# Performance work log

Hardware: AMD Instinct MI355X
Metric: run time of the kernel (lower is better)

## Reference

```python
import jax, jax.numpy as jnp
import numpy as np

BETA = 0.25
K = 4096


def setup_inputs() -> dict:
    key = jax.random.key(0)
    k1, k2 = jax.random.split(key)
    z = jax.random.normal(k1, (32, 256, 32, 32), dtype=jnp.float32)
    # matches torch init: uniform(-1/k, 1/k)
    embedding = jax.random.uniform(k2, (K, 256), dtype=jnp.float32,
                                   minval=-1.0 / K, maxval=1.0 / K)
    return {"z": z, "embedding": embedding}


def reference(z, embedding):
    b, d, h, w = z.shape
    k = embedding.shape[0]
    # (b d h w) -> (n d)
    z_flat = jnp.transpose(z, (0, 2, 3, 1)).reshape(-1, d)
    # squared euclidean distances, (n, k)
    distances = (jnp.sum(z_flat * z_flat, axis=-1, keepdims=True)
                 + jnp.sum(embedding * embedding, axis=-1)
                 - 2.0 * jnp.einsum('nd,kd->nk', z_flat, embedding))
    encoding_indices = jnp.argmin(distances, axis=1)
    encodings_onehot = jax.nn.one_hot(encoding_indices, k, dtype=z.dtype)
    zq_flat = embedding[encoding_indices]
    z_quantized = jnp.transpose(zq_flat.reshape(b, h, w, d), (0, 3, 1, 2))
    loss_encoder = jnp.mean((jax.lax.stop_gradient(z_quantized) - z) ** 2)
    loss_codebook = jnp.mean((z_quantized - jax.lax.stop_gradient(z)) ** 2)
    loss = BETA * loss_encoder + loss_codebook
    # straight-through estimator
    z_quantized_st = z + jax.lax.stop_gradient(z_quantized - z)
    # perplexity of codebook usage
    enc_mean = jnp.mean(encodings_onehot, axis=0)
    perplexity = jnp.exp(-jnp.sum(enc_mean * jnp.log(enc_mean + 1e-10)))
    return (z_quantized_st, loss, perplexity, encodings_onehot,
            encoding_indices, distances)
```

## Files before the change

### kernel.cpp

```cpp
#include <hip/hip_runtime.h>
#include <hip/hip_bf16.h>

typedef unsigned short u16;
typedef unsigned int u32;
typedef unsigned long long u64;
typedef __attribute__((ext_vector_type(8))) short bf16x8;
typedef __attribute__((ext_vector_type(4))) float f32x4;

#define NROWS 32768
#define KCODES 4096
#define DDIM 256
#define HW 1024
#define ZSTRIDE_B 262144ULL

#define OFF_ZQ   0ULL
#define OFF_LOSS 8388608ULL
#define OFF_PERP 8388609ULL
#define OFF_OH   8388610ULL
#define OFF_IDX  142606338ULL
#define OFF_DIST 142639106ULL

#define T_ZH 16777280ULL
#define T_EH 25165888ULL

#define WS_IDX    0
#define WS_COUNTS 131072
#define WS_EN2    147456
#define WS_ZN2    163840
#define WS_PART   294912
#define WS_BDIST  295424
#define WS_BMIN   524288

__global__ __launch_bounds__(64) void k_prep_e_en2(const float* __restrict__ emb,
                                                   float* __restrict__ en2,
                                                   u16* __restrict__ Ehh) {
    int k = blockIdx.x;
    int l = threadIdx.x;
    float4 v = *(const float4*)(emb + (size_t)k * DDIM + l * 4);
    float s = v.x * v.x + v.y * v.y + v.z * v.z + v.w * v.w;
    #pragma unroll
    for (int m = 32; m; m >>= 1) s += __shfl_xor(s, m);
    if (l == 0) en2[k] = s;
    float vv[4] = {v.x, v.y, v.z, v.w};
    u16 ho[4];
    #pragma unroll
    for (int j = 0; j < 4; ++j) {
        __hip_bfloat16 hb = __float2bfloat16(vv[j]);
        ho[j] = *(u16*)&hb;
    }
    *(ushort4*)(Ehh + (size_t)k * DDIM + l * 4) = make_ushort4(ho[0], ho[1], ho[2], ho[3]);
}

__global__ __launch_bounds__(256) void k_zn2(const float* __restrict__ z,
                                             float* __restrict__ zn2) {
    int n = blockIdx.x * 256 + threadIdx.x;
    int b = n >> 10, hw = n & 1023;
    const float* zp = z + (size_t)b * ZSTRIDE_B + hw;
    float s = 0.f;
    #pragma unroll 8
    for (int d = 0; d < DDIM; ++d) {
        float v = zp[(size_t)d * HW];
        s = fmaf(v, v, s);
    }
    zn2[n] = s;
}

__global__ __launch_bounds__(256) void k_prep_z(const float* __restrict__ z,
                                                u16* __restrict__ Zhh) {
    __shared__ float t[32][132];
    const int tid = threadIdx.x;
    const int h0 = blockIdx.x * 128, d0 = blockIdx.y * 32, b = blockIdx.z;
    const float* zp = z + (size_t)b * ZSTRIDE_B;
    {
        int hq = (tid & 31) << 2;
        int dr = tid >> 5;
        #pragma unroll
        for (int p = 0; p < 4; ++p) {
            int d = p * 8 + dr;
            float4 v = *(const float4*)(zp + (size_t)(d0 + d) * HW + h0 + hq);
            *(float4*)&t[d][hq] = v;
        }
    }
    __syncthreads();
    {
        int nr = tid >> 1;
        int half = tid & 1;
        int n = b * HW + h0 + nr;
        u16 hv[16];
        #pragma unroll
        for (int i = 0; i < 16; ++i) {
            float v = t[half * 16 + i][nr];
            __hip_bfloat16 hb = __float2bfloat16(v);
            hv[i] = *(u16*)&hb;
        }
        u16* dst = Zhh + (size_t)n * DDIM + d0 + half * 16;
        #pragma unroll
        for (int q = 0; q < 4; ++q)
            *(ushort4*)(dst + q * 4) = *(ushort4*)&hv[q * 4];
    }
}

__global__ __launch_bounds__(256) void k_dist_mfma(
    const u16* __restrict__ Zhh, const u16* __restrict__ Ehh,
    const float* __restrict__ zn2, const float* __restrict__ en2,
    float* __restrict__ dist, float* __restrict__ bmin)
{
    __shared__ __align__(16) u16 smem[16384];
    u16* As = smem;
    u16* Bs = smem + 8192;
    float* Ct = (float*)smem;

    const int tid = threadIdx.x;
    const int w = tid >> 6, l = tid & 63;
    const int n0 = blockIdx.x * 128, k0 = blockIdx.y * 128;
    const int kb = blockIdx.y;
    const int wr = w >> 1, wc = w & 1;

    int goff[4], loff[4];
    #pragma unroll
    for (int it = 0; it < 4; ++it) {
        int o = (it << 12) + (w << 10) + (l << 4);
        int r = o >> 7;
        int c16 = (o >> 4) & 7;
        int gs = c16 ^ (r & 7);
        goff[it] = r * DDIM + gs * 8;
        loff[it] = (it << 11) + (w << 9);
    }

    f32x4 acc[4][4];
    #pragma unroll
    for (int m = 0; m < 4; ++m)
        #pragma unroll
        for (int n = 0; n < 4; ++n)
            acc[m][n] = (f32x4){0.f, 0.f, 0.f, 0.f};

    const int lr = l & 15, ks = l >> 4;
    const int ra = wr * 64 + lr, rb = wc * 64 + lr;

    const u16* Ap = Zhh + (size_t)n0 * DDIM;
    const u16* Bp = Ehh + (size_t)k0 * DDIM;
    for (int st = 0; st < 4; ++st) {
        const int d0 = st * 64;
        #pragma unroll
        for (int it = 0; it < 4; ++it) {
            __builtin_amdgcn_global_load_lds(
                (const __attribute__((address_space(1))) void*)(Ap + d0 + goff[it]),
                (__attribute__((address_space(3))) void*)(As + loff[it]), 16, 0, 0);
            __builtin_amdgcn_global_load_lds(
                (const __attribute__((address_space(1))) void*)(Bp + d0 + goff[it]),
                (__attribute__((address_space(3))) void*)(Bs + loff[it]), 16, 0, 0);
        }
        __syncthreads();
        #pragma unroll
        for (int kk = 0; kk < 2; ++kk) {
            bf16x8 af[4], bfr[4];
            #pragma unroll
            for (int m = 0; m < 4; ++m) {
                int rr = ra + m * 16;
                af[m] = *(const bf16x8*)&As[rr * 64 + ((kk * 4 + ks) ^ (rr & 7)) * 8];
            }
            #pragma unroll
            for (int n = 0; n < 4; ++n) {
                int rr = rb + n * 16;
                bfr[n] = *(const bf16x8*)&Bs[rr * 64 + ((kk * 4 + ks) ^ (rr & 7)) * 8];
            }
            #pragma unroll
            for (int m = 0; m < 4; ++m)
                #pragma unroll
                for (int n = 0; n < 4; ++n)
                    acc[m][n] = __builtin_amdgcn_mfma_f32_16x16x32_bf16(
                        af[m], bfr[n], acc[m][n], 0, 0, 0);
        }
        __syncthreads();
    }

    float ev[4];
    #pragma unroll
    for (int n = 0; n < 4; ++n) ev[n] = en2[k0 + wc * 64 + n * 16 + lr];

    #pragma unroll
    for (int m = 0; m < 4; ++m) {
        #pragma unroll
        for (int r = 0; r < 4; ++r) {
            int row = n0 + wr * 64 + m * 16 + ks * 4 + r;
            float t = zn2[row];
            int ridx = wr * 16 + ks * 4 + r;
            float rm = 3.4e38f;
            #pragma unroll
            for (int n = 0; n < 4; ++n) {
                float s  = __fadd_rn(t, ev[n]);
                float m2 = __fmul_rn(2.0f, acc[m][n][r]);
                float dv = __fsub_rn(s, m2);
                Ct[ridx * 132 + wc * 64 + n * 16 + lr] = dv;
                rm = fminf(rm, dv);
            }
            #pragma unroll
            for (int msk = 1; msk < 16; msk <<= 1)
                rm = fminf(rm, __shfl_xor(rm, msk));
            if (lr == 0)
                bmin[((size_t)row * 32 + kb) * 2 + wc] = rm;
        }
        __syncthreads();
        #pragma unroll
        for (int rr = 0; rr < 8; ++rr) {
            int rid = w * 8 + rr;
            int grow = n0 + m * 16 + (rid >> 4) * 64 + (rid & 15);
            float a = Ct[rid * 132 + l * 2];
            float b = Ct[rid * 132 + l * 2 + 1];
            *(float2*)(dist + (size_t)grow * KCODES + k0 + l * 2) = make_float2(a, b);
        }
        __syncthreads();
    }
}

__global__ __launch_bounds__(256) void k_select(
    const float* __restrict__ dist, const float* __restrict__ z,
    const float* __restrict__ emb, const float* __restrict__ zn2,
    const float* __restrict__ en2, const float* __restrict__ bmin,
    u32* __restrict__ idxarr, float* __restrict__ bdist)
{
    const int l = threadIdx.x & 63;
    const int row = blockIdx.x * 4 + (threadIdx.x >> 6);
    float bm = bmin[(size_t)row * 64 + l];
    float mn = bm;
    #pragma unroll
    for (int m = 1; m < 64; m <<= 1) mn = fminf(mn, __shfl_xor(mn, m));
    const float thr = mn + 1e-3f;
    u64 qual = __ballot(bm <= thr);

    const int b = row >> 10, hw = row & 1023;
    const float* zp = z + (size_t)b * ZSTRIDE_B + hw;
    float z0 = zp[(size_t)(l * 4 + 0) * HW];
    float z1 = zp[(size_t)(l * 4 + 1) * HW];
    float z2 = zp[(size_t)(l * 4 + 2) * HW];
    float z3 = zp[(size_t)(l * 4 + 3) * HW];
    const float zr = zn2[row];

    u64 best = ~0ull;
    int prev_kb = -1;
    u64 qq = qual;
    while (qq) {
        int bit = __ffsll(qq) - 1; qq &= qq - 1;
        int kb = bit >> 1;
        if (kb == prev_kb) continue;
        prev_kb = kb;
        const float* dr = dist + (size_t)row * KCODES + kb * 128;
        float2 d2 = *(const float2*)(dr + l * 2);
        u64 c0 = __ballot(d2.x <= thr);
        u64 c1 = __ballot(d2.y <= thr);
        u64 any = c0 | c1;
        while (any) {
            int src = __ffsll(any) - 1; any &= any - 1;
            #pragma unroll
            for (int e = 0; e < 2; ++e) {
                u64 msk = e ? c1 : c0;
                if (!((msk >> src) & 1)) continue;
                int k = kb * 128 + src * 2 + e;
                float4 e4 = *(const float4*)(emb + (size_t)k * DDIM + l * 4);
                float p = 0.f;
                p = fmaf(z0, e4.x, p);
                p = fmaf(z1, e4.y, p);
                p = fmaf(z2, e4.z, p);
                p = fmaf(z3, e4.w, p);
                #pragma unroll
                for (int m = 1; m < 64; m <<= 1) p += __shfl_xor(p, m);
                float dh = __fsub_rn(__fadd_rn(zr, en2[k]), __fmul_rn(2.0f, p));
                u32 ub = __float_as_uint(dh);
                ub = (ub & 0x80000000u) ? ~ub : (ub | 0x80000000u);
                u64 cand = ((u64)ub << 32) | (u32)k;
                best = cand < best ? cand : best;
            }
        }
    }
    if (l == 0) {
        idxarr[row] = (u32)(best & 0xffffffffu);
        u32 ub = (u32)(best >> 32);
        u32 fb = (ub & 0x80000000u) ? (ub & 0x7fffffffu) : ~ub;
        bdist[row] = __uint_as_float(fb);
    }
}

__global__ __launch_bounds__(256) void k_zq(const float* __restrict__ emb,
                                            const u32* __restrict__ idxarr,
                                            const float* __restrict__ bdist,
                                            unsigned* __restrict__ counts,
                                            float* __restrict__ out,
                                            float* __restrict__ partials) {
    int n = blockIdx.x * 256 + threadIdx.x;
    unsigned idx = idxarr[n];
    out[OFF_IDX + n] = (float)idx;
    atomicAdd(counts + idx, 1u);
    int b = n >> 10, hw = n & 1023;
    const float* ep = emb + (size_t)idx * DDIM;
    float* oq = out + OFF_ZQ + (size_t)b * ZSTRIDE_B + hw;
    #pragma unroll 2
    for (int d = 0; d < DDIM; d += 4) {
        float4 e4 = *(const float4*)(ep + d);
        oq[(size_t)(d + 0) * HW] = e4.x;
        oq[(size_t)(d + 1) * HW] = e4.y;
        oq[(size_t)(d + 2) * HW] = e4.z;
        oq[(size_t)(d + 3) * HW] = e4.w;
    }
    __shared__ float red[256];
    red[threadIdx.x] = bdist[n];
    __syncthreads();
    for (int st = 128; st > 0; st >>= 1) {
        if (threadIdx.x < st) red[threadIdx.x] += red[threadIdx.x + st];
        __syncthreads();
    }
    if (threadIdx.x == 0) partials[blockIdx.x] = red[0];
}

__global__ __launch_bounds__(256) void k_onehot(const u32* __restrict__ idxarr,
                                                const unsigned* __restrict__ counts,
                                                const float* __restrict__ partials,
                                                float* __restrict__ out) {
    const int l = threadIdx.x & 63;
    const int n = blockIdx.x * 4 + (threadIdx.x >> 6);
    const int idx = (int)idxarr[n];
    float* base = out + OFF_OH + (size_t)n * KCODES;
    #pragma unroll
    for (int i = 0; i < 16; ++i) {
        int c0 = i * 256 + l * 4;
        float2 a, b2;
        a.x  = (idx == c0)     ? 1.0f : 0.0f;
        a.y  = (idx == c0 + 1) ? 1.0f : 0.0f;
        b2.x = (idx == c0 + 2) ? 1.0f : 0.0f;
        b2.y = (idx == c0 + 3) ? 1.0f : 0.0f;
        *(float2*)(base + c0) = a;
        *(float2*)(base + c0 + 2) = b2;
    }
    if (blockIdx.x == 0) {
        __shared__ float red[256];
        int t = threadIdx.x;
        red[t] = (t < 128) ? partials[t] : 0.f;
        __syncthreads();
        for (int st = 128; st > 0; st >>= 1) {
            if (t < st) red[t] += red[t + st];
            __syncthreads();
        }
        float loss = 1.25f * (red[0] / 8388608.0f);
        __syncthreads();
        float h = 0.f;
        for (int k = t; k < KCODES; k += 256) {
            float p = (float)counts[k] * (1.0f / 32768.0f);
            h -= p * logf(p + 1e-10f);
        }
        red[t] = h;
        __syncthreads();
        for (int st = 128; st > 0; st >>= 1) {
            if (t < st) red[t] += red[t + st];
            __syncthreads();
        }
        if (t == 0) {
            out[OFF_LOSS] = loss;
            out[OFF_PERP] = expf(red[0]);
        }
    }
}

extern "C" void kernel_launch(void* const* d_in, const int* in_sizes, int n_in,
                              void* d_out, int out_size, void* d_ws, size_t ws_size,
                              hipStream_t stream) {
    (void)in_sizes; (void)n_in; (void)out_size; (void)ws_size;
    const float* z = (const float*)d_in[0];
    const float* emb = (const float*)d_in[1];
    float* out = (float*)d_out;
    char* ws = (char*)d_ws;
    u32* idxarr = (u32*)(ws + WS_IDX);
    unsigned* counts = (unsigned*)(ws + WS_COUNTS);
    float* en2 = (float*)(ws + WS_EN2);
    float* zn2 = (float*)(ws + WS_ZN2);
    float* partials = (float*)(ws + WS_PART);
    float* bdist = (float*)(ws + WS_BDIST);
    float* bmin = (float*)(ws + WS_BMIN);

    u16* Zhh = (u16*)(out + T_ZH);
    u16* Ehh = (u16*)(out + T_EH);
    float* dist = out + OFF_DIST;

    (void)hipMemsetAsync(counts, 0, (size_t)KCODES * 4, stream);

    k_prep_z<<<dim3(8, 8, 32), 256, 0, stream>>>(z, Zhh);
    k_prep_e_en2<<<KCODES, 64, 0, stream>>>(emb, en2, Ehh);
    k_zn2<<<NROWS / 256, 256, 0, stream>>>(z, zn2);
    k_dist_mfma<<<dim3(NROWS / 128, KCODES / 128), 256, 0, stream>>>(
        Zhh, Ehh, zn2, en2, dist, bmin);
    k_select<<<NROWS / 4, 256, 0, stream>>>(dist, z, emb, zn2, en2, bmin,
                                            idxarr, bdist);
    k_zq<<<NROWS / 256, 256, 0, stream>>>(emb, idxarr, bdist, counts, out, partials);
    k_onehot<<<NROWS / 4, 256, 0, stream>>>(idxarr, counts, partials, out);
}
```

Measured before the change: 554.6 us.

## Keep Z tile resident in LDS across four codebook panels and overlap epilogue

Each block of the distance GEMM now loads its full 128x256 Z tile into LDS once and loops over four 128-code panels, so Z is fetched from global memory a quarter as often and the grid shrinks to a quarter of its former size. The previous panel's epilogue is issued after the next panel's first B loads, overlapping distance writes with loads. The epilogue now writes distances straight to global memory from MFMA registers instead of staging them through LDS for coalesced float2 stores. This gives less coalesced stores and uses 80KB of LDS per block, which limits occupancy.

```diff
diff --git a/kernel.cpp b/kernel.cpp
--- a/kernel.cpp
+++ b/kernel.cpp
@@ -100,98 +100,28 @@
     }
 }
 
-__global__ __launch_bounds__(256) void k_dist_mfma(
-    const u16* __restrict__ Zhh, const u16* __restrict__ Ehh,
-    const float* __restrict__ zn2, const float* __restrict__ en2,
-    float* __restrict__ dist, float* __restrict__ bmin)
+static __device__ __forceinline__ void do_epilogue(
+    f32x4 (&acc)[4][4], const float* zrow, const float* __restrict__ en2,
+    float* __restrict__ dist, float* __restrict__ bmin,
+    int n0, int kpan, int kb, int wr, int wc, int lr, int ks)
 {
-    __shared__ __align__(16) u16 smem[16384];
-    u16* As = smem;
-    u16* Bs = smem + 8192;
-    float* Ct = (float*)smem;
-
-    const int tid = threadIdx.x;
-    const int w = tid >> 6, l = tid & 63;
-    const int n0 = blockIdx.x * 128, k0 = blockIdx.y * 128;
-    const int kb = blockIdx.y;
-    const int wr = w >> 1, wc = w & 1;
-
-    int goff[4], loff[4];
-    #pragma unroll
-    for (int it = 0; it < 4; ++it) {
-        int o = (it << 12) + (w << 10) + (l << 4);
-        int r = o >> 7;
-        int c16 = (o >> 4) & 7;
-        int gs = c16 ^ (r & 7);
-        goff[it] = r * DDIM + gs * 8;
-        loff[it] = (it << 11) + (w << 9);
-    }
-
-    f32x4 acc[4][4];
-    #pragma unroll
-    for (int m = 0; m < 4; ++m)
-        #pragma unroll
-        for (int n = 0; n < 4; ++n)
-            acc[m][n] = (f32x4){0.f, 0.f, 0.f, 0.f};
-
-    const int lr = l & 15, ks = l >> 4;
-    const int ra = wr * 64 + lr, rb = wc * 64 + lr;
-
-    const u16* Ap = Zhh + (size_t)n0 * DDIM;
-    const u16* Bp = Ehh + (size_t)k0 * DDIM;
-    for (int st = 0; st < 4; ++st) {
-        const int d0 = st * 64;
-        #pragma unroll
-        for (int it = 0; it < 4; ++it) {
-            __builtin_amdgcn_global_load_lds(
-                (const __attribute__((address_space(1))) void*)(Ap + d0 + goff[it]),
-                (__attribute__((address_space(3))) void*)(As + loff[it]), 16, 0, 0);
-            __builtin_amdgcn_global_load_lds(
-                (const __attribute__((address_space(1))) void*)(Bp + d0 + goff[it]),
-                (__attribute__((address_space(3))) void*)(Bs + loff[it]), 16, 0, 0);
-        }
-        __syncthreads();
-        #pragma unroll
-        for (int kk = 0; kk < 2; ++kk) {
-            bf16x8 af[4], bfr[4];
-            #pragma unroll
-            for (int m = 0; m < 4; ++m) {
-                int rr = ra + m * 16;
-                af[m] = *(const bf16x8*)&As[rr * 64 + ((kk * 4 + ks) ^ (rr & 7)) * 8];
-            }
-            #pragma unroll
-            for (int n = 0; n < 4; ++n) {
-                int rr = rb + n * 16;
-                bfr[n] = *(const bf16x8*)&Bs[rr * 64 + ((kk * 4 + ks) ^ (rr & 7)) * 8];
-            }
-            #pragma unroll
-            for (int m = 0; m < 4; ++m)
-                #pragma unroll
-                for (int n = 0; n < 4; ++n)
-                    acc[m][n] = __builtin_amdgcn_mfma_f32_16x16x32_bf16(
-                        af[m], bfr[n], acc[m][n], 0, 0, 0);
-        }
-        __syncthreads();
-    }
-
     float ev[4];
     #pragma unroll
-    for (int n = 0; n < 4; ++n) ev[n] = en2[k0 + wc * 64 + n * 16 + lr];
-
+    for (int n = 0; n < 4; ++n) ev[n] = en2[kpan + wc * 64 + n * 16 + lr];
     #pragma unroll
     for (int m = 0; m < 4; ++m) {
         #pragma unroll
         for (int r = 0; r < 4; ++r) {
             int row = n0 + wr * 64 + m * 16 + ks * 4 + r;
-            float t = zn2[row];
-            int ridx = wr * 16 + ks * 4 + r;
+            float t = zrow[m * 4 + r];
+            float* dp = dist + (size_t)row * KCODES + kpan + wc * 64 + lr;
             float rm = 3.4e38f;
             #pragma unroll
             for (int n = 0; n < 4; ++n) {
                 float s  = __fadd_rn(t, ev[n]);
                 float m2 = __fmul_rn(2.0f, acc[m][n][r]);
                 float dv = __fsub_rn(s, m2);
-                Ct[ridx * 132 + wc * 64 + n * 16 + lr] = dv;
+                dp[n * 16] = dv;
                 rm = fminf(rm, dv);
             }
             #pragma unroll
@@ -200,17 +130,103 @@
             if (lr == 0)
                 bmin[((size_t)row * 32 + kb) * 2 + wc] = rm;
         }
-        __syncthreads();
-        #pragma unroll
-        for (int rr = 0; rr < 8; ++rr) {
-            int rid = w * 8 + rr;
-            int grow = n0 + m * 16 + (rid >> 4) * 64 + (rid & 15);
-            float a = Ct[rid * 132 + l * 2];
-            float b = Ct[rid * 132 + l * 2 + 1];
-            *(float2*)(dist + (size_t)grow * KCODES + k0 + l * 2) = make_float2(a, b);
-        }
-        __syncthreads();
-    }
+        #pragma unroll
+        for (int n = 0; n < 4; ++n) acc[m][n] = (f32x4){0.f, 0.f, 0.f, 0.f};
+    }
+}
+
+__global__ __launch_bounds__(256) void k_dist_mfma(
+    const u16* __restrict__ Zhh, const u16* __restrict__ Ehh,
+    const float* __restrict__ zn2, const float* __restrict__ en2,
+    float* __restrict__ dist, float* __restrict__ bmin)
+{
+    __shared__ __align__(16) u16 As[32768];
+    __shared__ __align__(16) u16 Bs[8192];
+
+    const int tid = threadIdx.x;
+    const int w = tid >> 6, l = tid & 63;
+    const int n0 = blockIdx.x * 128;
+    const int kbase = blockIdx.y * 512;
+    const int wr = w >> 1, wc = w & 1;
+    const int lr = l & 15, ks = l >> 4;
+    const int ra = wr * 64 + lr, rb = wc * 64 + lr;
+
+    int goff[4], loff[4];
+    #pragma unroll
+    for (int it = 0; it < 4; ++it) {
+        int o = (it << 12) + (w << 10) + (l << 4);
+        int r = o >> 7;
+        int gs = ((o >> 4) & 7) ^ (r & 7);
+        goff[it] = r * DDIM + gs * 8;
+        loff[it] = (it << 11) + (w << 9);
+    }
+
+    const u16* Ap = Zhh + (size_t)n0 * DDIM;
+    #pragma unroll
+    for (int c = 0; c < 4; ++c)
+        #pragma unroll
+        for (int it = 0; it < 4; ++it)
+            __builtin_amdgcn_global_load_lds(
+                (const __attribute__((address_space(1))) void*)(Ap + c * 64 + goff[it]),
+                (__attribute__((address_space(3))) void*)(As + c * 8192 + loff[it]),
+                16, 0, 0);
+
+    f32x4 acc[4][4];
+    #pragma unroll
+    for (int m = 0; m < 4; ++m)
+        #pragma unroll
+        for (int n = 0; n < 4; ++n)
+            acc[m][n] = (f32x4){0.f, 0.f, 0.f, 0.f};
+
+    float zrow[16];
+    #pragma unroll
+    for (int m = 0; m < 4; ++m)
+        #pragma unroll
+        for (int r = 0; r < 4; ++r)
+            zrow[m * 4 + r] = zn2[n0 + wr * 64 + m * 16 + ks * 4 + r];
+
+    for (int p = 0; p < 4; ++p) {
+        const int kpan = kbase + p * 128;
+        const u16* Bp = Ehh + (size_t)kpan * DDIM;
+        for (int st = 0; st < 4; ++st) {
+            #pragma unroll
+            for (int it = 0; it < 4; ++it)
+                __builtin_amdgcn_global_load_lds(
+                    (const __attribute__((address_space(1))) void*)(Bp + st * 64 + goff[it]),
+                    (__attribute__((address_space(3))) void*)(Bs + loff[it]),
+                    16, 0, 0);
+            if (st == 0 && p > 0) {
+                do_epilogue(acc, zrow, en2, dist, bmin, n0, kpan - 128,
+                            blockIdx.y * 4 + p - 1, wr, wc, lr, ks);
+            }
+            __syncthreads();
+            #pragma unroll
+            for (int kk = 0; kk < 2; ++kk) {
+                bf16x8 af[4], bfr[4];
+                #pragma unroll
+                for (int m = 0; m < 4; ++m) {
+                    int rr = ra + m * 16;
+                    af[m] = *(const bf16x8*)&As[st * 8192 + rr * 64 +
+                                                ((kk * 4 + ks) ^ (rr & 7)) * 8];
+                }
+                #pragma unroll
+                for (int n = 0; n < 4; ++n) {
+                    int rr = rb + n * 16;
+                    bfr[n] = *(const bf16x8*)&Bs[rr * 64 +
+                                                 ((kk * 4 + ks) ^ (rr & 7)) * 8];
+                }
+                #pragma unroll
+                for (int m = 0; m < 4; ++m)
+                    #pragma unroll
+                    for (int n = 0; n < 4; ++n)
+                        acc[m][n] = __builtin_amdgcn_mfma_f32_16x16x32_bf16(
+                            af[m], bfr[n], acc[m][n], 0, 0, 0);
+            }
+            __syncthreads();
+        }
+    }
+    do_epilogue(acc, zrow, en2, dist, bmin, n0, kbase + 384,
+                blockIdx.y * 4 + 3, wr, wc, lr, ks);
 }
 
 __global__ __launch_bounds__(256) void k_select(
@@ -384,7 +400,7 @@
     k_prep_z<<<dim3(8, 8, 32), 256, 0, stream>>>(z, Zhh);
     k_prep_e_en2<<<KCODES, 64, 0, stream>>>(emb, en2, Ehh);
     k_zn2<<<NROWS / 256, 256, 0, stream>>>(z, zn2);
-    k_dist_mfma<<<dim3(NROWS / 128, KCODES / 128), 256, 0, stream>>>(
+    k_dist_mfma<<<dim3(NROWS / 128, KCODES / 512), 256, 0, stream>>>(
         Zhh, Ehh, zn2, en2, dist, bmin);
     k_select<<<NROWS / 4, 256, 0, stream>>>(dist, z, emb, zn2, en2, bmin,
                                             idxarr, bdist);
```

Measured after the change: 631.8 us. 13.9% more time.

## Load MFMA operands directly from global memory instead of staging through LDS

Applied to the files above, without the earlier changes.

The distance GEMM kernel stops staging Z and codebook tiles in shared memory with global_load_lds and barriers. Each wave now reads its bf16 fragments straight from global memory, relying on L1/L2 for reuse. The shared buffer shrinks to the epilogue transpose, and the launch bounds ask for three blocks per CU. The goal is to drop barrier and LDS overhead and raise occupancy, at the cost of redundant global/L2 traffic because the two waves sharing a row or column block each fetch it.

```diff
diff --git a/kernel.cpp b/kernel.cpp
--- a/kernel.cpp
+++ b/kernel.cpp
@@ -100,32 +100,22 @@
     }
 }
 
-__global__ __launch_bounds__(256) void k_dist_mfma(
+__global__ __launch_bounds__(256, 3) void k_dist_mfma(
     const u16* __restrict__ Zhh, const u16* __restrict__ Ehh,
     const float* __restrict__ zn2, const float* __restrict__ en2,
     float* __restrict__ dist, float* __restrict__ bmin)
 {
-    __shared__ __align__(16) u16 smem[16384];
-    u16* As = smem;
-    u16* Bs = smem + 8192;
-    float* Ct = (float*)smem;
+    __shared__ __align__(16) float Ct[32 * 132];
 
     const int tid = threadIdx.x;
     const int w = tid >> 6, l = tid & 63;
     const int n0 = blockIdx.x * 128, k0 = blockIdx.y * 128;
     const int kb = blockIdx.y;
     const int wr = w >> 1, wc = w & 1;
-
-    int goff[4], loff[4];
-    #pragma unroll
-    for (int it = 0; it < 4; ++it) {
-        int o = (it << 12) + (w << 10) + (l << 4);
-        int r = o >> 7;
-        int c16 = (o >> 4) & 7;
-        int gs = c16 ^ (r & 7);
-        goff[it] = r * DDIM + gs * 8;
-        loff[it] = (it << 11) + (w << 9);
-    }
+    const int lr = l & 15, ks = l >> 4;
+
+    const u16* Ap = Zhh + (size_t)(n0 + wr * 64 + lr) * DDIM + ks * 8;
+    const u16* Bp = Ehh + (size_t)(k0 + wc * 64 + lr) * DDIM + ks * 8;
 
     f32x4 acc[4][4];
     #pragma unroll
@@ -134,36 +124,18 @@
         for (int n = 0; n < 4; ++n)
             acc[m][n] = (f32x4){0.f, 0.f, 0.f, 0.f};
 
-    const int lr = l & 15, ks = l >> 4;
-    const int ra = wr * 64 + lr, rb = wc * 64 + lr;
-
-    const u16* Ap = Zhh + (size_t)n0 * DDIM;
-    const u16* Bp = Ehh + (size_t)k0 * DDIM;
+    #pragma unroll
     for (int st = 0; st < 4; ++st) {
-        const int d0 = st * 64;
-        #pragma unroll
-        for (int it = 0; it < 4; ++it) {
-            __builtin_amdgcn_global_load_lds(
-                (const __attribute__((address_space(1))) void*)(Ap + d0 + goff[it]),
-                (__attribute__((address_space(3))) void*)(As + loff[it]), 16, 0, 0);
-            __builtin_amdgcn_global_load_lds(
-                (const __attribute__((address_space(1))) void*)(Bp + d0 + goff[it]),
-                (__attribute__((address_space(3))) void*)(Bs + loff[it]), 16, 0, 0);
-        }
-        __syncthreads();
         #pragma unroll
         for (int kk = 0; kk < 2; ++kk) {
+            const int off = st * 64 + kk * 32;
             bf16x8 af[4], bfr[4];
             #pragma unroll
-            for (int m = 0; m < 4; ++m) {
-                int rr = ra + m * 16;
-                af[m] = *(const bf16x8*)&As[rr * 64 + ((kk * 4 + ks) ^ (rr & 7)) * 8];
-            }
-            #pragma unroll
-            for (int n = 0; n < 4; ++n) {
-                int rr = rb + n * 16;
-                bfr[n] = *(const bf16x8*)&Bs[rr * 64 + ((kk * 4 + ks) ^ (rr & 7)) * 8];
-            }
+            for (int m = 0; m < 4; ++m)
+                af[m] = *(const bf16x8*)(Ap + (size_t)m * 16 * DDIM + off);
+            #pragma unroll
+            for (int n = 0; n < 4; ++n)
+                bfr[n] = *(const bf16x8*)(Bp + (size_t)n * 16 * DDIM + off);
             #pragma unroll
             for (int m = 0; m < 4; ++m)
                 #pragma unroll
@@ -171,7 +143,6 @@
                     acc[m][n] = __builtin_amdgcn_mfma_f32_16x16x32_bf16(
                         af[m], bfr[n], acc[m][n], 0, 0, 0);
         }
-        __syncthreads();
     }
 
     float ev[4];
```

Result: slower. 640.4 us (+15.5%).
